# Optimization experiments

Hardware: AMD Instinct MI355X
Metric: run time of the kernel (lower is better)

## Reference

```python
import jax, jax.numpy as jnp
import numpy as np

SCALE = 0.08838834764831845  # 1/sqrt(128)

def setup_inputs() -> dict:
    key = jax.random.key(0)
    k1, k2 = jax.random.split(key)
    x1 = jax.random.normal(k1, (16, 2048, 128), dtype=jnp.float32)
    x2 = jax.random.normal(k2, (16, 2048, 128), dtype=jnp.float32)
    return {"x1": x1, "x2": x2}

def reference(x1, x2):
    # qk = x1 @ x2^T  -> [B, Lq, Lk]
    qk = jnp.einsum('bqd,bkd->bqk', x1, x2) * SCALE
    attn = jax.nn.softmax(qk, axis=-1)
    # dropout p=0.0 -> identity
    # output = attn @ x2 (x2 doubles as values in the source module)
    out = jnp.einsum('bqk,bkd->bqd', attn, x2)
    return out
```

## Files before the change

### kernel.cpp

```cpp
#include <hip/hip_runtime.h>
#include <hip/hip_bf16.h>

typedef __attribute__((ext_vector_type(8))) short bf16x8;
typedef __attribute__((ext_vector_type(4))) float f32x4;
typedef __attribute__((ext_vector_type(4))) unsigned u32x4;
typedef __attribute__((ext_vector_type(2))) unsigned u32x2;

#define NSEQ 2048
#define DH 128
#define QBLK 64
#define KVB 64
#define QSCALE 0.12751744716167933f
#define DEFER_THR 8.0f
#define KVSTRIDE 32768

__device__ __forceinline__ unsigned cvtpk(float lo, float hi) {
  unsigned r;
  asm("v_cvt_pk_bf16_f32 %0, %1, %2" : "=v"(r) : "v"(lo), "v"(hi));
  return r;
}
__device__ __forceinline__ float fexp2(float x) { return __builtin_amdgcn_exp2f(x); }

__device__ __forceinline__ int swzT(int d) {
  return ((d & 7) ^ ((d >> 3) & 7)) << 4;
}

__global__ __launch_bounds__(256, 2) void attn_fwd(
    const float* __restrict__ x1, const float* __restrict__ x2,
    float* __restrict__ out) {
  __shared__ char lds[73728];
  char* plds = lds + 65536;

  const int tid = threadIdx.x;
  const int lane = tid & 63;
  const int wid = tid >> 6;
  const int g = lane >> 4;
  const int q15 = lane & 15;

  const int bb = blockIdx.y;
  const int qbase = blockIdx.x * QBLK + wid * 16;

  const float* x1b = x1 + (size_t)bb * NSEQ * DH;
  const float* x2b = x2 + (size_t)bb * NSEQ * DH;

  u32x4 qf[4];
  {
    const float* qp = x1b + (size_t)(qbase + q15) * DH + g * 8;
#pragma unroll
    for (int c = 0; c < 4; ++c) {
      f32x4 v0 = *(const f32x4*)(qp + c * 32);
      f32x4 v1 = *(const f32x4*)(qp + c * 32 + 4);
      u32x4 w;
      w[0] = cvtpk(v0[0] * QSCALE, v0[1] * QSCALE);
      w[1] = cvtpk(v0[2] * QSCALE, v0[3] * QSCALE);
      w[2] = cvtpk(v1[0] * QSCALE, v1[1] * QSCALE);
      w[3] = cvtpk(v1[2] * QSCALE, v1[3] * QSCALE);
      qf[c] = w;
    }
  }

  const int kgrp = tid >> 4;
  const int dg = tid & 15;
  f32x4 ra[4][2];

  auto LOADRA = [&](int kv0) {
    if (kv0 < NSEQ) {
#pragma unroll
      for (int p = 0; p < 4; ++p) {
        const float* s = x2b + (size_t)(kv0 + kgrp * 4 + p) * DH + dg * 8;
        ra[p][0] = *(const f32x4*)s;
        ra[p][1] = *(const f32x4*)(s + 4);
      }
    }
  };

  auto WRITELDS = [&](int b) {
    char* kvAb = lds + b * KVSTRIDE;
    char* kvTb = kvAb + 16384;
#pragma unroll
    for (int p = 0; p < 4; ++p) {
      u32x4 w;
      w[0] = cvtpk(ra[p][0][0], ra[p][0][1]);
      w[1] = cvtpk(ra[p][0][2], ra[p][0][3]);
      w[2] = cvtpk(ra[p][1][0], ra[p][1][1]);
      w[3] = cvtpk(ra[p][1][2], ra[p][1][3]);
      const int key = kgrp * 4 + p;
      *(u32x4*)(kvAb + key * 256 + ((dg * 16) ^ ((key & 7) << 4))) = w;
    }
#pragma unroll
    for (int h = 0; h < 2; ++h)
#pragma unroll
      for (int ii = 0; ii < 4; ++ii) {
        const int d = dg * 8 + h * 4 + ii;
        u32x2 cw;
        cw[0] = cvtpk(ra[0][h][ii], ra[1][h][ii]);
        cw[1] = cvtpk(ra[2][h][ii], ra[3][h][ii]);
        *(u32x2*)(kvTb + d * 128 + ((kgrp * 8) ^ swzT(d))) = cw;
      }
  };

  float m_run = -1e30f;
  float l_run = 0.f;
  f32x4 o[8];
#pragma unroll
  for (int dc = 0; dc < 8; ++dc) o[dc] = (f32x4){0.f, 0.f, 0.f, 0.f};

  LOADRA(0);
  WRITELDS(0);
  LOADRA(KVB);
  asm volatile("s_waitcnt lgkmcnt(0)" ::: "memory");
  __builtin_amdgcn_s_barrier();
  int cur = 0;

  for (int kv0 = 0; kv0 < NSEQ; kv0 += KVB) {
    char* kvA = lds + cur * KVSTRIDE;
    char* kvT = kvA + 16384;

    f32x4 sf[4];
#pragma unroll
    for (int kb = 0; kb < 4; ++kb) {
      sf[kb] = (f32x4){0.f, 0.f, 0.f, 0.f};
      const int key = kb * 16 + q15;
#pragma unroll
      for (int c = 0; c < 4; ++c) {
        bf16x8 a = *(const bf16x8*)(kvA + key * 256 +
                                    ((c * 64 + g * 16) ^ ((key & 7) << 4)));
        sf[kb] = __builtin_amdgcn_mfma_f32_16x16x32_bf16(
            a, *(const bf16x8*)&qf[c], sf[kb], 0, 0, 0);
      }
    }

    float mloc = -1e30f;
#pragma unroll
    for (int kb = 0; kb < 4; ++kb)
#pragma unroll
      for (int r = 0; r < 4; ++r) mloc = fmaxf(mloc, sf[kb][r]);
    mloc = fmaxf(mloc, __shfl_xor(mloc, 16));
    mloc = fmaxf(mloc, __shfl_xor(mloc, 32));
    if (!__all(mloc <= m_run + DEFER_THR)) {
      const float mnew = fmaxf(m_run, mloc);
      const float corr = fexp2(m_run - mnew);
#pragma unroll
      for (int r = 0; r < 4; ++r) {
        const float fr = __shfl(corr, g * 4 + r);
#pragma unroll
        for (int dc = 0; dc < 8; ++dc) o[dc][r] *= fr;
      }
      l_run *= corr;
      m_run = mnew;
    }
    float tsum = 0.f;
    float pf[4][4];
#pragma unroll
    for (int kb = 0; kb < 4; ++kb)
#pragma unroll
      for (int r = 0; r < 4; ++r) {
        const float pv = fexp2(sf[kb][r] - m_run);
        tsum += pv;
        pf[kb][r] = pv;
      }
    tsum += __shfl_xor(tsum, 16);
    tsum += __shfl_xor(tsum, 32);
    l_run += tsum;

    if (kv0 + KVB < NSEQ) {
      WRITELDS(cur ^ 1);
      LOADRA(kv0 + 2 * KVB);
    }

#pragma unroll
    for (int kb = 0; kb < 4; ++kb) {
      u32x2 pw;
      pw[0] = cvtpk(pf[kb][0], pf[kb][1]);
      pw[1] = cvtpk(pf[kb][2], pf[kb][3]);
      *(u32x2*)(plds + wid * 2048 + q15 * 128 +
                ((kb * 32 + g * 8) ^ ((q15 & 7) << 4))) = pw;
    }

#pragma unroll
    for (int kc = 0; kc < 2; ++kc) {
      bf16x8 pa = *(const bf16x8*)(plds + wid * 2048 + q15 * 128 +
                                   ((kc * 64 + g * 16) ^ ((q15 & 7) << 4)));
#pragma unroll
      for (int dc = 0; dc < 8; ++dc) {
        const int d = dc * 16 + q15;
        bf16x8 vb = *(const bf16x8*)(kvT + d * 128 +
                                     ((kc * 64 + g * 16) ^ swzT(d)));
        o[dc] = __builtin_amdgcn_mfma_f32_16x16x32_bf16(pa, vb, o[dc], 0, 0, 0);
      }
    }

    asm volatile("s_waitcnt lgkmcnt(0)" ::: "memory");
    __builtin_amdgcn_s_barrier();
    cur ^= 1;
  }

#pragma unroll
  for (int r = 0; r < 4; ++r) {
    const float linv = 1.0f / __shfl(l_run, g * 4 + r);
    const int q = qbase + g * 4 + r;
    float* op = out + (size_t)bb * NSEQ * DH + (size_t)q * DH + q15;
#pragma unroll
    for (int dc = 0; dc < 8; ++dc) op[dc * 16] = o[dc][r] * linv;
  }
}

extern "C" void kernel_launch(void* const* d_in, const int* in_sizes, int n_in,
                              void* d_out, int out_size, void* d_ws, size_t ws_size,
                              hipStream_t stream) {
  const float* x1 = (const float*)d_in[0];
  const float* x2 = (const float*)d_in[1];
  float* out = (float*)d_out;
  dim3 grid(NSEQ / QBLK, 16);
  attn_fwd<<<grid, dim3(256), 0, stream>>>(x1, x2, out);
}
```

Baseline: 134.4 us.

## Process two 16-row query tiles per wave to double K/V reuse

Each wave now handles 32 query rows as two 16-row sub-tiles, so every K/V fragment read from LDS feeds two MFMAs and the block covers 128 queries, halving the grid and the global K/V traffic per query. The PV MFMA operands are swapped so the output accumulator is laid out with query rows along lanes, which removes the per-row shuffles for the rescale and allows vectorized float4 output stores. The cost is more registers (occupancy hint reduced to 1 block per CU), a larger LDS footprint, and only 256 blocks, which may underfill the GPU.

```diff
diff --git a/kernel.cpp b/kernel.cpp
--- a/kernel.cpp
+++ b/kernel.cpp
@@ -8,7 +8,7 @@
 
 #define NSEQ 2048
 #define DH 128
-#define QBLK 64
+#define QBLK 128
 #define KVB 64
 #define QSCALE 0.12751744716167933f
 #define DEFER_THR 8.0f
@@ -25,10 +25,10 @@
   return ((d & 7) ^ ((d >> 3) & 7)) << 4;
 }
 
-__global__ __launch_bounds__(256, 2) void attn_fwd(
+__global__ __launch_bounds__(256, 1) void attn_fwd(
     const float* __restrict__ x1, const float* __restrict__ x2,
     float* __restrict__ out) {
-  __shared__ char lds[73728];
+  __shared__ char lds[81920];
   char* plds = lds + 65536;
 
   const int tid = threadIdx.x;
@@ -38,14 +38,15 @@
   const int q15 = lane & 15;
 
   const int bb = blockIdx.y;
-  const int qbase = blockIdx.x * QBLK + wid * 16;
+  const int qbase = blockIdx.x * QBLK + wid * 32;
 
   const float* x1b = x1 + (size_t)bb * NSEQ * DH;
   const float* x2b = x2 + (size_t)bb * NSEQ * DH;
 
-  u32x4 qf[4];
-  {
-    const float* qp = x1b + (size_t)(qbase + q15) * DH + g * 8;
+  u32x4 qf[2][4];
+#pragma unroll
+  for (int s = 0; s < 2; ++s) {
+    const float* qp = x1b + (size_t)(qbase + s * 16 + q15) * DH + g * 8;
 #pragma unroll
     for (int c = 0; c < 4; ++c) {
       f32x4 v0 = *(const f32x4*)(qp + c * 32);
@@ -55,7 +56,7 @@
       w[1] = cvtpk(v0[2] * QSCALE, v0[3] * QSCALE);
       w[2] = cvtpk(v1[0] * QSCALE, v1[1] * QSCALE);
       w[3] = cvtpk(v1[2] * QSCALE, v1[3] * QSCALE);
-      qf[c] = w;
+      qf[s][c] = w;
     }
   }
 
@@ -99,11 +100,13 @@
       }
   };
 
-  float m_run = -1e30f;
-  float l_run = 0.f;
-  f32x4 o[8];
-#pragma unroll
-  for (int dc = 0; dc < 8; ++dc) o[dc] = (f32x4){0.f, 0.f, 0.f, 0.f};
+  float m_run[2] = {-1e30f, -1e30f};
+  float l_run[2] = {0.f, 0.f};
+  f32x4 o[2][8];
+#pragma unroll
+  for (int s = 0; s < 2; ++s)
+#pragma unroll
+    for (int dc = 0; dc < 8; ++dc) o[s][dc] = (f32x4){0.f, 0.f, 0.f, 0.f};
 
   LOADRA(0);
   WRITELDS(0);
@@ -116,52 +119,72 @@
     char* kvA = lds + cur * KVSTRIDE;
     char* kvT = kvA + 16384;
 
-    f32x4 sf[4];
+    f32x4 sf[2][4];
 #pragma unroll
     for (int kb = 0; kb < 4; ++kb) {
-      sf[kb] = (f32x4){0.f, 0.f, 0.f, 0.f};
+      sf[0][kb] = (f32x4){0.f, 0.f, 0.f, 0.f};
+      sf[1][kb] = (f32x4){0.f, 0.f, 0.f, 0.f};
       const int key = kb * 16 + q15;
 #pragma unroll
       for (int c = 0; c < 4; ++c) {
         bf16x8 a = *(const bf16x8*)(kvA + key * 256 +
                                     ((c * 64 + g * 16) ^ ((key & 7) << 4)));
-        sf[kb] = __builtin_amdgcn_mfma_f32_16x16x32_bf16(
-            a, *(const bf16x8*)&qf[c], sf[kb], 0, 0, 0);
-      }
-    }
-
-    float mloc = -1e30f;
-#pragma unroll
-    for (int kb = 0; kb < 4; ++kb)
-#pragma unroll
-      for (int r = 0; r < 4; ++r) mloc = fmaxf(mloc, sf[kb][r]);
-    mloc = fmaxf(mloc, __shfl_xor(mloc, 16));
-    mloc = fmaxf(mloc, __shfl_xor(mloc, 32));
-    if (!__all(mloc <= m_run + DEFER_THR)) {
-      const float mnew = fmaxf(m_run, mloc);
-      const float corr = fexp2(m_run - mnew);
-#pragma unroll
-      for (int r = 0; r < 4; ++r) {
-        const float fr = __shfl(corr, g * 4 + r);
-#pragma unroll
-        for (int dc = 0; dc < 8; ++dc) o[dc][r] *= fr;
-      }
-      l_run *= corr;
-      m_run = mnew;
-    }
-    float tsum = 0.f;
-    float pf[4][4];
-#pragma unroll
-    for (int kb = 0; kb < 4; ++kb)
-#pragma unroll
-      for (int r = 0; r < 4; ++r) {
-        const float pv = fexp2(sf[kb][r] - m_run);
-        tsum += pv;
-        pf[kb][r] = pv;
-      }
-    tsum += __shfl_xor(tsum, 16);
-    tsum += __shfl_xor(tsum, 32);
-    l_run += tsum;
+        sf[0][kb] = __builtin_amdgcn_mfma_f32_16x16x32_bf16(
+            a, *(const bf16x8*)&qf[0][c], sf[0][kb], 0, 0, 0);
+        sf[1][kb] = __builtin_amdgcn_mfma_f32_16x16x32_bf16(
+            a, *(const bf16x8*)&qf[1][c], sf[1][kb], 0, 0, 0);
+      }
+    }
+
+    float mloc[2];
+#pragma unroll
+    for (int s = 0; s < 2; ++s) {
+      float m = -1e30f;
+#pragma unroll
+      for (int kb = 0; kb < 4; ++kb)
+#pragma unroll
+        for (int r = 0; r < 4; ++r) m = fmaxf(m, sf[s][kb][r]);
+      m = fmaxf(m, __shfl_xor(m, 16));
+      m = fmaxf(m, __shfl_xor(m, 32));
+      mloc[s] = m;
+    }
+    const bool ok = (mloc[0] <= m_run[0] + DEFER_THR) &&
+                    (mloc[1] <= m_run[1] + DEFER_THR);
+    if (!__all(ok)) {
+#pragma unroll
+      for (int s = 0; s < 2; ++s) {
+        const float mnew = fmaxf(m_run[s], mloc[s]);
+        const float corr = fexp2(m_run[s] - mnew);
+#pragma unroll
+        for (int dc = 0; dc < 8; ++dc) o[s][dc] *= corr;
+        l_run[s] *= corr;
+        m_run[s] = mnew;
+      }
+    }
+#pragma unroll
+    for (int s = 0; s < 2; ++s) {
+      float tsum = 0.f;
+      float pf[4][4];
+#pragma unroll
+      for (int kb = 0; kb < 4; ++kb)
+#pragma unroll
+        for (int r = 0; r < 4; ++r) {
+          const float pv = fexp2(sf[s][kb][r] - m_run[s]);
+          tsum += pv;
+          pf[kb][r] = pv;
+        }
+      tsum += __shfl_xor(tsum, 16);
+      tsum += __shfl_xor(tsum, 32);
+      l_run[s] += tsum;
+#pragma unroll
+      for (int kb = 0; kb < 4; ++kb) {
+        u32x2 pw;
+        pw[0] = cvtpk(pf[kb][0], pf[kb][1]);
+        pw[1] = cvtpk(pf[kb][2], pf[kb][3]);
+        *(u32x2*)(plds + wid * 4096 + s * 2048 + q15 * 128 +
+                  ((kb * 32 + g * 8) ^ ((q15 & 7) << 4))) = pw;
+      }
+    }
 
     if (kv0 + KVB < NSEQ) {
       WRITELDS(cur ^ 1);
@@ -169,24 +192,18 @@
     }
 
 #pragma unroll
-    for (int kb = 0; kb < 4; ++kb) {
-      u32x2 pw;
-      pw[0] = cvtpk(pf[kb][0], pf[kb][1]);
-      pw[1] = cvtpk(pf[kb][2], pf[kb][3]);
-      *(u32x2*)(plds + wid * 2048 + q15 * 128 +
-                ((kb * 32 + g * 8) ^ ((q15 & 7) << 4))) = pw;
-    }
-
-#pragma unroll
     for (int kc = 0; kc < 2; ++kc) {
-      bf16x8 pa = *(const bf16x8*)(plds + wid * 2048 + q15 * 128 +
-                                   ((kc * 64 + g * 16) ^ ((q15 & 7) << 4)));
+      bf16x8 pa0 = *(const bf16x8*)(plds + wid * 4096 + q15 * 128 +
+                                    ((kc * 64 + g * 16) ^ ((q15 & 7) << 4)));
+      bf16x8 pa1 = *(const bf16x8*)(plds + wid * 4096 + 2048 + q15 * 128 +
+                                    ((kc * 64 + g * 16) ^ ((q15 & 7) << 4)));
 #pragma unroll
       for (int dc = 0; dc < 8; ++dc) {
         const int d = dc * 16 + q15;
         bf16x8 vb = *(const bf16x8*)(kvT + d * 128 +
                                      ((kc * 64 + g * 16) ^ swzT(d)));
-        o[dc] = __builtin_amdgcn_mfma_f32_16x16x32_bf16(pa, vb, o[dc], 0, 0, 0);
+        o[0][dc] = __builtin_amdgcn_mfma_f32_16x16x32_bf16(vb, pa0, o[0][dc], 0, 0, 0);
+        o[1][dc] = __builtin_amdgcn_mfma_f32_16x16x32_bf16(vb, pa1, o[1][dc], 0, 0, 0);
       }
     }
 
@@ -196,12 +213,14 @@
   }
 
 #pragma unroll
-  for (int r = 0; r < 4; ++r) {
-    const float linv = 1.0f / __shfl(l_run, g * 4 + r);
-    const int q = qbase + g * 4 + r;
-    float* op = out + (size_t)bb * NSEQ * DH + (size_t)q * DH + q15;
-#pragma unroll
-    for (int dc = 0; dc < 8; ++dc) op[dc * 16] = o[dc][r] * linv;
+  for (int s = 0; s < 2; ++s) {
+    const float linv = 1.0f / l_run[s];
+    float* op = out + (size_t)bb * NSEQ * DH + (size_t)(qbase + s * 16 + q15) * DH;
+#pragma unroll
+    for (int dc = 0; dc < 8; ++dc) {
+      f32x4 v = o[s][dc] * linv;
+      *(f32x4*)(op + dc * 16 + g * 4) = v;
+    }
   }
 }
 
```

Result: faster. 130.7 us (-2.8%).

## Keep P in registers via permuted K layout and double Q block to 8 waves

Applied to the files above, without the earlier changes.

Grows the query block to 128 rows with 512 threads, so each staged K/V tile is shared by twice as many queries and per-thread staging work is halved. K rows are written to LDS in a permuted order so that the QK^T MFMA output layout matches the A-operand layout needed for PV. This lets P stay in registers instead of round-tripping through LDS, and the P scratch buffer is dropped. The PV MFMA operands are swapped so the output is transposed, which makes the rescale a per-lane scalar and allows vectorized output stores. The larger block raises register and occupancy pressure under launch_bounds(512,2) and halves the grid size.

```diff
diff --git a/kernel.cpp b/kernel.cpp
--- a/kernel.cpp
+++ b/kernel.cpp
@@ -4,15 +4,14 @@
 typedef __attribute__((ext_vector_type(8))) short bf16x8;
 typedef __attribute__((ext_vector_type(4))) float f32x4;
 typedef __attribute__((ext_vector_type(4))) unsigned u32x4;
-typedef __attribute__((ext_vector_type(2))) unsigned u32x2;
 
 #define NSEQ 2048
 #define DH 128
-#define QBLK 64
+#define QBLK 128
 #define KVB 64
 #define QSCALE 0.12751744716167933f
 #define DEFER_THR 8.0f
-#define KVSTRIDE 32768
+#define KVBUF 32768
 
 __device__ __forceinline__ unsigned cvtpk(float lo, float hi) {
   unsigned r;
@@ -21,15 +20,20 @@
 }
 __device__ __forceinline__ float fexp2(float x) { return __builtin_amdgcn_exp2f(x); }
 
+__device__ __forceinline__ void wg_barrier() {
+  asm volatile("s_waitcnt lgkmcnt(0)" ::: "memory");
+  __builtin_amdgcn_s_barrier();
+  asm volatile("" ::: "memory");
+}
+
 __device__ __forceinline__ int swzT(int d) {
   return ((d & 7) ^ ((d >> 3) & 7)) << 4;
 }
 
-__global__ __launch_bounds__(256, 2) void attn_fwd(
+__global__ __launch_bounds__(512, 2) void attn_fwd(
     const float* __restrict__ x1, const float* __restrict__ x2,
     float* __restrict__ out) {
-  __shared__ char lds[73728];
-  char* plds = lds + 65536;
+  __shared__ char lds[65536];
 
   const int tid = threadIdx.x;
   const int lane = tid & 63;
@@ -59,15 +63,15 @@
     }
   }
 
-  const int kgrp = tid >> 4;
+  const int kg = tid >> 4;
   const int dg = tid & 15;
-  f32x4 ra[4][2];
+  f32x4 ra[2][2];
 
   auto LOADRA = [&](int kv0) {
     if (kv0 < NSEQ) {
 #pragma unroll
-      for (int p = 0; p < 4; ++p) {
-        const float* s = x2b + (size_t)(kv0 + kgrp * 4 + p) * DH + dg * 8;
+      for (int p = 0; p < 2; ++p) {
+        const float* s = x2b + (size_t)(kv0 + kg * 2 + p) * DH + dg * 8;
         ra[p][0] = *(const f32x4*)s;
         ra[p][1] = *(const f32x4*)(s + 4);
       }
@@ -75,27 +79,26 @@
   };
 
   auto WRITELDS = [&](int b) {
-    char* kvAb = lds + b * KVSTRIDE;
+    char* kvAb = lds + b * KVBUF;
     char* kvTb = kvAb + 16384;
 #pragma unroll
-    for (int p = 0; p < 4; ++p) {
+    for (int p = 0; p < 2; ++p) {
       u32x4 w;
       w[0] = cvtpk(ra[p][0][0], ra[p][0][1]);
       w[1] = cvtpk(ra[p][0][2], ra[p][0][3]);
       w[2] = cvtpk(ra[p][1][0], ra[p][1][1]);
       w[3] = cvtpk(ra[p][1][2], ra[p][1][3]);
-      const int key = kgrp * 4 + p;
-      *(u32x4*)(kvAb + key * 256 + ((dg * 16) ^ ((key & 7) << 4))) = w;
+      const int key = kg * 2 + p;
+      const int rho = (key & 0x23) | ((key & 4) << 2) | ((key & 0x18) >> 1);
+      *(u32x4*)(kvAb + rho * 256 + ((dg * 16) ^ ((rho & 7) << 4))) = w;
     }
 #pragma unroll
     for (int h = 0; h < 2; ++h)
 #pragma unroll
       for (int ii = 0; ii < 4; ++ii) {
         const int d = dg * 8 + h * 4 + ii;
-        u32x2 cw;
-        cw[0] = cvtpk(ra[0][h][ii], ra[1][h][ii]);
-        cw[1] = cvtpk(ra[2][h][ii], ra[3][h][ii]);
-        *(u32x2*)(kvTb + d * 128 + ((kgrp * 8) ^ swzT(d))) = cw;
+        const unsigned cw = cvtpk(ra[0][h][ii], ra[1][h][ii]);
+        *(unsigned*)(kvTb + d * 128 + ((kg * 4) ^ swzT(d))) = cw;
       }
   };
 
@@ -108,23 +111,22 @@
   LOADRA(0);
   WRITELDS(0);
   LOADRA(KVB);
-  asm volatile("s_waitcnt lgkmcnt(0)" ::: "memory");
-  __builtin_amdgcn_s_barrier();
+  wg_barrier();
   int cur = 0;
 
   for (int kv0 = 0; kv0 < NSEQ; kv0 += KVB) {
-    char* kvA = lds + cur * KVSTRIDE;
+    char* kvA = lds + cur * KVBUF;
     char* kvT = kvA + 16384;
 
     f32x4 sf[4];
 #pragma unroll
     for (int kb = 0; kb < 4; ++kb) {
       sf[kb] = (f32x4){0.f, 0.f, 0.f, 0.f};
-      const int key = kb * 16 + q15;
+      const int row = kb * 16 + q15;
 #pragma unroll
       for (int c = 0; c < 4; ++c) {
-        bf16x8 a = *(const bf16x8*)(kvA + key * 256 +
-                                    ((c * 64 + g * 16) ^ ((key & 7) << 4)));
+        bf16x8 a = *(const bf16x8*)(kvA + row * 256 +
+                                    ((c * 64 + g * 16) ^ ((row & 7) << 4)));
         sf[kb] = __builtin_amdgcn_mfma_f32_16x16x32_bf16(
             a, *(const bf16x8*)&qf[c], sf[kb], 0, 0, 0);
       }
@@ -141,11 +143,7 @@
       const float mnew = fmaxf(m_run, mloc);
       const float corr = fexp2(m_run - mnew);
 #pragma unroll
-      for (int r = 0; r < 4; ++r) {
-        const float fr = __shfl(corr, g * 4 + r);
-#pragma unroll
-        for (int dc = 0; dc < 8; ++dc) o[dc][r] *= fr;
-      }
+      for (int dc = 0; dc < 8; ++dc) o[dc] *= corr;
       l_run *= corr;
       m_run = mnew;
     }
@@ -162,6 +160,16 @@
     tsum += __shfl_xor(tsum, 16);
     tsum += __shfl_xor(tsum, 32);
     l_run += tsum;
+    u32x4 pa[2];
+#pragma unroll
+    for (int kc = 0; kc < 2; ++kc) {
+      u32x4 w;
+      w[0] = cvtpk(pf[2 * kc][0], pf[2 * kc][1]);
+      w[1] = cvtpk(pf[2 * kc][2], pf[2 * kc][3]);
+      w[2] = cvtpk(pf[2 * kc + 1][0], pf[2 * kc + 1][1]);
+      w[3] = cvtpk(pf[2 * kc + 1][2], pf[2 * kc + 1][3]);
+      pa[kc] = w;
+    }
 
     if (kv0 + KVB < NSEQ) {
       WRITELDS(cur ^ 1);
@@ -169,39 +177,29 @@
     }
 
 #pragma unroll
-    for (int kb = 0; kb < 4; ++kb) {
-      u32x2 pw;
-      pw[0] = cvtpk(pf[kb][0], pf[kb][1]);
-      pw[1] = cvtpk(pf[kb][2], pf[kb][3]);
-      *(u32x2*)(plds + wid * 2048 + q15 * 128 +
-                ((kb * 32 + g * 8) ^ ((q15 & 7) << 4))) = pw;
-    }
-
-#pragma unroll
     for (int kc = 0; kc < 2; ++kc) {
-      bf16x8 pa = *(const bf16x8*)(plds + wid * 2048 + q15 * 128 +
-                                   ((kc * 64 + g * 16) ^ ((q15 & 7) << 4)));
 #pragma unroll
       for (int dc = 0; dc < 8; ++dc) {
         const int d = dc * 16 + q15;
         bf16x8 vb = *(const bf16x8*)(kvT + d * 128 +
                                      ((kc * 64 + g * 16) ^ swzT(d)));
-        o[dc] = __builtin_amdgcn_mfma_f32_16x16x32_bf16(pa, vb, o[dc], 0, 0, 0);
-      }
-    }
-
-    asm volatile("s_waitcnt lgkmcnt(0)" ::: "memory");
-    __builtin_amdgcn_s_barrier();
+        o[dc] = __builtin_amdgcn_mfma_f32_16x16x32_bf16(
+            vb, *(const bf16x8*)&pa[kc], o[dc], 0, 0, 0);
+      }
+    }
+
+    wg_barrier();
     cur ^= 1;
   }
 
-#pragma unroll
-  for (int r = 0; r < 4; ++r) {
-    const float linv = 1.0f / __shfl(l_run, g * 4 + r);
-    const int q = qbase + g * 4 + r;
-    float* op = out + (size_t)bb * NSEQ * DH + (size_t)q * DH + q15;
-#pragma unroll
-    for (int dc = 0; dc < 8; ++dc) op[dc * 16] = o[dc][r] * linv;
+  {
+    const float linv = 1.0f / l_run;
+    float* op = out + (size_t)bb * NSEQ * DH + (size_t)(qbase + q15) * DH;
+#pragma unroll
+    for (int dc = 0; dc < 8; ++dc) {
+      f32x4 v = o[dc] * linv;
+      *(f32x4*)(op + dc * 16 + g * 4) = v;
+    }
   }
 }
 
@@ -212,5 +210,5 @@
   const float* x2 = (const float*)d_in[1];
   float* out = (float*)d_out;
   dim3 grid(NSEQ / QBLK, 16);
-  attn_fwd<<<grid, dim3(256), 0, stream>>>(x1, x2, out);
-}
+  attn_fwd<<<grid, dim3(512), 0, stream>>>(x1, x2, out);
+}
```

After: 127.3 us. 1.06x faster.
